# Kernel tuning notes

Hardware: AMD Instinct MI355X
Metric: run time of the kernel (lower is better)

## Reference

```python
import jax, jax.numpy as jnp
import numpy as np

EPS = 1e-8

def rmsnorm(x, w):
    norm = jax.lax.rsqrt(jnp.mean(x * x, axis=-1, keepdims=True) + EPS)
    return x * norm * w

def setup_inputs() -> dict:
    key = jax.random.key(0)
    ks = jax.random.split(key, 10)
    B, L, D, S = 8, 4096, 1024, 256
    sD = 1.0 / np.sqrt(D)
    sS = 1.0 / np.sqrt(S)
    return {
        "x": jax.random.normal(ks[0], (B, L, D), jnp.float32),
        "w_norm": jnp.ones((D,), jnp.float32),
        "W_in": jax.random.normal(ks[1], (D, 3 * S), jnp.float32) * sD,
        "b_in": jnp.zeros((3 * S,), jnp.float32),
        "W_x": jax.random.normal(ks[2], (S, S), jnp.float32) * sS,
        "b_x": jnp.zeros((S,), jnp.float32),
        "W_dt": jax.random.normal(ks[3], (S, S), jnp.float32) * sS,
        "b_dt": jnp.zeros((S,), jnp.float32),
        "W_out": jax.random.normal(ks[4], (S, D), jnp.float32) * sS,
        "b_out": jnp.zeros((D,), jnp.float32),
    }

def reference(x, w_norm, W_in, b_in, W_x, b_x, W_dt, b_dt, W_out, b_out):
    # MambaLikeBlock forward (dropout=0 / eval mode)
    residual = x
    xn = rmsnorm(x, w_norm)
    uzg = xn @ W_in + b_in                       # [B,L,3S]
    S = uzg.shape[-1] // 3
    u, z, g = uzg[..., :S], uzg[..., S:2 * S], uzg[..., 2 * S:]
    # per-step projections are time-independent -> precompute for all t
    ut = jnp.tanh(u @ W_x + b_x)                 # [B,L,S]
    dt = jax.nn.sigmoid(z @ W_dt + b_dt)         # [B,L,S]

    def step(h, inp):
        u_t, dt_t = inp
        h = (1.0 - dt_t) * h + dt_t * u_t
        return h, h

    h0 = jnp.zeros(ut.shape[::2][::-1][:0] + (ut.shape[0], ut.shape[2]), ut.dtype)  # [B,S]
    _, hs = jax.lax.scan(step, h0, (ut.transpose(1, 0, 2), dt.transpose(1, 0, 2)))
    hs = hs.transpose(1, 0, 2)                   # [B,L,S]
    y = hs * jax.nn.sigmoid(g)
    y = y @ W_out + b_out                        # [B,L,D]
    return residual + y
```

## Files before the change

kernel.cpp:

```cpp
#include <hip/hip_runtime.h>
#include <hip/hip_bf16.h>

#define BB 8
#define LL 4096
#define DD 1024
#define SS 256
#define NTOK (BB * LL)
#define CCH 64
#define TCH (LL / CCH)

typedef short bf16x8 __attribute__((ext_vector_type(8)));
typedef float f32x4 __attribute__((ext_vector_type(4)));

__device__ __forceinline__ float bfu(unsigned short v) {
  union { unsigned int i; float f; } x;
  x.i = ((unsigned int)v) << 16;
  return x.f;
}

__device__ __forceinline__ void gl_lds16(const __hip_bfloat16* g, void* l) {
  __builtin_amdgcn_global_load_lds(
      (const __attribute__((address_space(1))) unsigned int*)g,
      (__attribute__((address_space(3))) unsigned int*)l, 16, 0, 0);
}

__global__ __launch_bounds__(256) void prep_rms(const float* __restrict__ x,
                                                const float* __restrict__ wn,
                                                __hip_bfloat16* __restrict__ xn) {
  const size_t row = blockIdx.x;
  const int t = threadIdx.x;
  const float4 xv = reinterpret_cast<const float4*>(x + row * DD)[t];
  const float4 wv = reinterpret_cast<const float4*>(wn)[t];
  float ss = xv.x * xv.x + xv.y * xv.y + xv.z * xv.z + xv.w * xv.w;
#pragma unroll
  for (int m = 32; m >= 1; m >>= 1) ss += __shfl_xor(ss, m);
  __shared__ float red[4];
  if ((t & 63) == 0) red[t >> 6] = ss;
  __syncthreads();
  const float tot = red[0] + red[1] + red[2] + red[3];
  const float r = rsqrtf(tot * (1.0f / DD) + 1e-8f);
  union { ushort4 u; __hip_bfloat16 h[4]; } o;
  o.h[0] = __float2bfloat16(xv.x * wv.x * r);
  o.h[1] = __float2bfloat16(xv.y * wv.y * r);
  o.h[2] = __float2bfloat16(xv.z * wv.z * r);
  o.h[3] = __float2bfloat16(xv.w * wv.w * r);
  reinterpret_cast<ushort4*>(xn + row * DD)[t] = o.u;
}

__global__ __launch_bounds__(256) void convT4(
    const float* __restrict__ W0, const float* __restrict__ W1,
    const float* __restrict__ W2, const float* __restrict__ W3,
    __hip_bfloat16* __restrict__ T0, __hip_bfloat16* __restrict__ T1,
    __hip_bfloat16* __restrict__ T2, __hip_bfloat16* __restrict__ T3) {
  const int seg = blockIdx.y;
  const int K = (seg == 0) ? DD : SS;
  const int Nw = (seg == 0) ? 768 : (seg == 3) ? DD : SS;
  const float* W = (seg == 0) ? W0 : (seg == 1) ? W1 : (seg == 2) ? W2 : W3;
  __hip_bfloat16* T = (seg == 0) ? T0 : (seg == 1) ? T1 : (seg == 2) ? T2 : T3;
  const int idx = blockIdx.x * 256 + threadIdx.x;
  if (idx >= K * Nw) return;
  const int k = idx / Nw, n = idx % Nw;
  T[(size_t)n * K + k] = __float2bfloat16(W[idx]);
}

template <int EPI>
__global__ __launch_bounds__(256, 2) void gemm_bf16(
    const __hip_bfloat16* __restrict__ A, int lda,
    const __hip_bfloat16* __restrict__ BT,
    const float* __restrict__ bias,
    void* __restrict__ Cptr, int ldc,
    const float* __restrict__ resid,
    int K,
    const __hip_bfloat16* __restrict__ BT2,
    const float* __restrict__ bias2,
    void* __restrict__ Cptr2) {
  __shared__ __align__(16) char ldsA[2][128 * 128];
  __shared__ __align__(16) char ldsB[2][128 * 128];

  const int t = threadIdx.x;
  const int bm = blockIdx.x;
  const int bn = blockIdx.y;
  const int wave = t >> 6, lane = t & 63;
  const int wr = (wave >> 1) * 64;
  const int wc = (wave & 1) * 64;
  const int lr = lane & 15;
  const int kg = lane >> 4;
  const int rsw = lr & 7;

  const int which = (EPI == 4) ? (bn >> 1) : 0;
  const int bneff = (EPI == 4) ? (bn & 1) : bn;
  const __hip_bfloat16* Aeff = (EPI == 4 && which) ? A + SS : A;
  const __hip_bfloat16* BTeff = (EPI == 4 && which) ? BT2 : BT;
  const float* biaseff = (EPI == 4 && which) ? bias2 : bias;
  void* Ceff = (EPI == 4 && which) ? Cptr2 : Cptr;

  const int srow = lane >> 3;
  const int sg = (lane & 7) ^ srow;
  const int g_row = wave * 32 + srow;
  const __hip_bfloat16* Ab = Aeff + (size_t)(bm * 128 + g_row) * lda + sg * 8;
  const __hip_bfloat16* Bb = BTeff + (size_t)(bneff * 128 + g_row) * K + sg * 8;

  f32x4 acc[4][4] = {};

#define STAGE(d, koff)                                                        \
  {                                                                           \
    _Pragma("unroll") for (int p = 0; p < 4; ++p) {                           \
      gl_lds16(Ab + (size_t)(p * 8) * lda + (koff),                           \
               ldsA[d] + (wave * 32 + p * 8) * 128);                          \
      gl_lds16(Bb + (size_t)(p * 8) * K + (koff),                             \
               ldsB[d] + (wave * 32 + p * 8) * 128);                          \
    }                                                                         \
  }

  const int NT = K >> 6;
  STAGE(0, 0);

  for (int ti = 0; ti < NT; ++ti) {
    const int cur = ti & 1;
    if (ti + 1 < NT) {
      STAGE(cur ^ 1, (ti + 1) * 64);
      asm volatile("s_waitcnt vmcnt(8)" ::: "memory");
    } else {
      asm volatile("s_waitcnt vmcnt(0)" ::: "memory");
    }
    __builtin_amdgcn_sched_barrier(0);
    __builtin_amdgcn_s_barrier();
#pragma unroll
    for (int kh = 0; kh < 2; ++kh) {
      bf16x8 af[4], bfr[4];
#pragma unroll
      for (int m = 0; m < 4; ++m) {
        const int row = wr + m * 16 + lr;
        const int slot = (kg + kh * 4) ^ rsw;
        af[m] = *reinterpret_cast<const bf16x8*>(ldsA[cur] + row * 128 + slot * 16);
      }
#pragma unroll
      for (int n = 0; n < 4; ++n) {
        const int row = wc + n * 16 + lr;
        const int slot = (kg + kh * 4) ^ rsw;
        bfr[n] = *reinterpret_cast<const bf16x8*>(ldsB[cur] + row * 128 + slot * 16);
      }
#pragma unroll
      for (int m = 0; m < 4; ++m)
#pragma unroll
        for (int n = 0; n < 4; ++n)
          acc[m][n] = __builtin_amdgcn_mfma_f32_16x16x32_bf16(bfr[n], af[m],
                                                              acc[m][n], 0, 0, 0);
    }
    __builtin_amdgcn_sched_barrier(0);
    __builtin_amdgcn_s_barrier();
  }
#undef STAGE

  const int row0 = bm * 128 + wr + lr;
  const int col0 = bneff * 128 + wc + kg * 4;

  if (EPI == 3) {
    f32x4 rv[4][4];
    f32x4 bv[4];
#pragma unroll
    for (int n = 0; n < 4; ++n)
      bv[n] = *reinterpret_cast<const f32x4*>(&bias[col0 + n * 16]);
#pragma unroll
    for (int m = 0; m < 4; ++m) {
      const size_t rowoff = (size_t)(row0 + m * 16) * ldc;
#pragma unroll
      for (int n = 0; n < 4; ++n) {
        rv[m][n] = __builtin_nontemporal_load(
            reinterpret_cast<const f32x4*>(&resid[rowoff + col0 + n * 16]));
      }
    }
    __builtin_amdgcn_sched_barrier(0);
#pragma unroll
    for (int m = 0; m < 4; ++m) {
      const size_t rowoff = (size_t)(row0 + m * 16) * ldc;
#pragma unroll
      for (int n = 0; n < 4; ++n) {
        f32x4 ov = acc[m][n] + bv[n] + rv[m][n];
        *reinterpret_cast<f32x4*>(&((float*)Cptr)[rowoff + col0 + n * 16]) = ov;
      }
    }
  } else {
#pragma unroll
    for (int m = 0; m < 4; ++m) {
      const int row = row0 + m * 16;
#pragma unroll
      for (int n = 0; n < 4; ++n) {
        const int colb = col0 + n * 16;
        const float4 bvv = *reinterpret_cast<const float4*>(&biaseff[colb]);
        float v0 = acc[m][n][0] + bvv.x;
        float v1 = acc[m][n][1] + bvv.y;
        float v2 = acc[m][n][2] + bvv.z;
        float v3 = acc[m][n][3] + bvv.w;
        if (EPI == 1 || (EPI == 4 && which == 0)) {
          v0 = tanhf(v0); v1 = tanhf(v1); v2 = tanhf(v2); v3 = tanhf(v3);
        } else if (EPI == 2 || (EPI == 4 && which == 1)) {
          v0 = 1.f / (1.f + expf(-v0)); v1 = 1.f / (1.f + expf(-v1));
          v2 = 1.f / (1.f + expf(-v2)); v3 = 1.f / (1.f + expf(-v3));
        }
        union { ushort4 u; __hip_bfloat16 h[4]; } o;
        o.h[0] = __float2bfloat16(v0); o.h[1] = __float2bfloat16(v1);
        o.h[2] = __float2bfloat16(v2); o.h[3] = __float2bfloat16(v3);
        *reinterpret_cast<ushort4*>(
            &((__hip_bfloat16*)Ceff)[(size_t)row * ldc + colb]) = o.u;
      }
    }
  }
}

__global__ __launch_bounds__(128) void scan_phase_a(
    const __hip_bfloat16* __restrict__ ut,
    const __hip_bfloat16* __restrict__ dtb,
    float* __restrict__ h0s, float* __restrict__ As) {
  const int bc = blockIdx.x;
  const int b = bc / CCH, c = bc % CCH;
  const int ch = threadIdx.x * 2;
  const size_t base = ((size_t)b * LL + (size_t)c * TCH) * SS + ch;
  float h0 = 0.f, h1 = 0.f, A0 = 1.f, A1 = 1.f;
#pragma unroll 8
  for (int t = 0; t < TCH; ++t) {
    const ushort2 uu = *reinterpret_cast<const ushort2*>(ut + base + (size_t)t * SS);
    const ushort2 dd = *reinterpret_cast<const ushort2*>(dtb + base + (size_t)t * SS);
    const float d0 = bfu(dd.x), d1 = bfu(dd.y);
    h0 = fmaf(d0, bfu(uu.x) - h0, h0);
    h1 = fmaf(d1, bfu(uu.y) - h1, h1);
    A0 *= (1.f - d0);
    A1 *= (1.f - d1);
  }
  const size_t o = (size_t)bc * SS + ch;
  *reinterpret_cast<float2*>(h0s + o) = make_float2(h0, h1);
  *reinterpret_cast<float2*>(As + o) = make_float2(A0, A1);
}

__global__ __launch_bounds__(256) void scan_phase_b(
    const float* __restrict__ h0s, const float* __restrict__ As,
    float* __restrict__ hins) {
  const int b = blockIdx.x;
  const int s = threadIdx.x;
  float hin = 0.f;
#pragma unroll 8
  for (int c = 0; c < CCH; ++c) {
    const size_t idx = ((size_t)b * CCH + c) * SS + s;
    hins[idx] = hin;
    hin = fmaf(As[idx], hin, h0s[idx]);
  }
}

__global__ __launch_bounds__(128) void scan_phase_c(
    const __hip_bfloat16* __restrict__ ut,
    const __hip_bfloat16* __restrict__ dtb,
    const __hip_bfloat16* __restrict__ gz,
    const float* __restrict__ hins,
    __hip_bfloat16* __restrict__ hsg) {
  const int bc = blockIdx.x;
  const int b = bc / CCH, c = bc % CCH;
  const int ch = threadIdx.x * 2;
  const size_t rowbase = (size_t)b * LL + (size_t)c * TCH;
  const float2 hv = *reinterpret_cast<const float2*>(hins + (size_t)bc * SS + ch);
  float h0 = hv.x, h1 = hv.y;
#pragma unroll 8
  for (int t = 0; t < TCH; ++t) {
    const size_t row = rowbase + t;
    const ushort2 uu = *reinterpret_cast<const ushort2*>(ut + row * SS + ch);
    const ushort2 dd = *reinterpret_cast<const ushort2*>(dtb + row * SS + ch);
    const ushort2 gg = *reinterpret_cast<const ushort2*>(gz + row * 768 + ch);
    h0 = fmaf(bfu(dd.x), bfu(uu.x) - h0, h0);
    h1 = fmaf(bfu(dd.y), bfu(uu.y) - h1, h1);
    union { ushort2 u; __hip_bfloat16 h[2]; } o;
    o.h[0] = __float2bfloat16(h0 / (1.f + expf(-bfu(gg.x))));
    o.h[1] = __float2bfloat16(h1 / (1.f + expf(-bfu(gg.y))));
    *reinterpret_cast<ushort2*>(hsg + row * SS + ch) = o.u;
  }
}

extern "C" void kernel_launch(void* const* d_in, const int* in_sizes, int n_in,
                              void* d_out, int out_size, void* d_ws, size_t ws_size,
                              hipStream_t stream) {
  const float* x      = (const float*)d_in[0];
  const float* w_norm = (const float*)d_in[1];
  const float* W_in   = (const float*)d_in[2];
  const float* b_in   = (const float*)d_in[3];
  const float* W_x    = (const float*)d_in[4];
  const float* b_x    = (const float*)d_in[5];
  const float* W_dt   = (const float*)d_in[6];
  const float* b_dt   = (const float*)d_in[7];
  const float* W_out  = (const float*)d_in[8];
  const float* b_out  = (const float*)d_in[9];
  float* out = (float*)d_out;

  char* w = (char*)d_ws;
  __hip_bfloat16* xn  = (__hip_bfloat16*)w;
  __hip_bfloat16* ut  = (__hip_bfloat16*)w;
  __hip_bfloat16* dtb = (__hip_bfloat16*)(w + (size_t)NTOK * SS * 2);
  w += (size_t)NTOK * DD * 2;
  __hip_bfloat16* uzg = (__hip_bfloat16*)w;  w += (size_t)NTOK * 768 * 2;
  __hip_bfloat16* WinT  = (__hip_bfloat16*)w;  w += (size_t)768 * DD * 2;
  __hip_bfloat16* WxT   = (__hip_bfloat16*)w;  w += (size_t)SS * SS * 2;
  __hip_bfloat16* WdtT  = (__hip_bfloat16*)w;  w += (size_t)SS * SS * 2;
  __hip_bfloat16* WoutT = (__hip_bfloat16*)w;  w += (size_t)DD * SS * 2;
  float* h0s  = (float*)w;  w += (size_t)BB * CCH * SS * 4;
  float* As   = (float*)w;  w += (size_t)BB * CCH * SS * 4;
  float* hins = (float*)w;  w += (size_t)BB * CCH * SS * 4;
  (void)ws_size; (void)n_in; (void)in_sizes; (void)out_size;

  convT4<<<dim3((DD * 768 + 255) / 256, 4), 256, 0, stream>>>(
      W_in, W_x, W_dt, W_out, WinT, WxT, WdtT, WoutT);

  prep_rms<<<NTOK, 256, 0, stream>>>(x, w_norm, xn);

  gemm_bf16<0><<<dim3(NTOK / 128, 768 / 128), 256, 0, stream>>>(
      xn, DD, WinT, b_in, uzg, 768, nullptr, DD, nullptr, nullptr, nullptr);

  gemm_bf16<4><<<dim3(NTOK / 128, 4), 256, 0, stream>>>(
      uzg, 768, WxT, b_x, ut, SS, nullptr, SS, WdtT, b_dt, dtb);

  scan_phase_a<<<BB * CCH, 128, 0, stream>>>(ut, dtb, h0s, As);
  scan_phase_b<<<BB, 256, 0, stream>>>(h0s, As, hins);
  scan_phase_c<<<BB * CCH, 128, 0, stream>>>(ut, dtb, uzg + 2 * SS, hins, ut);

  gemm_bf16<3><<<dim3(NTOK / 128, DD / 128), 256, 0, stream>>>(
      ut, SS, WoutT, b_out, out, DD, x, SS, nullptr, nullptr, nullptr);
}
```

Measured before the change: 275.4 us.

## Switch GEMM to 4-stage K=32 LDS pipeline with three tiles in flight

```diff
diff --git a/kernel.cpp b/kernel.cpp
--- a/kernel.cpp
+++ b/kernel.cpp
@@ -74,8 +74,8 @@
     const __hip_bfloat16* __restrict__ BT2,
     const float* __restrict__ bias2,
     void* __restrict__ Cptr2) {
-  __shared__ __align__(16) char ldsA[2][128 * 128];
-  __shared__ __align__(16) char ldsB[2][128 * 128];
+  __shared__ __align__(16) char ldsA[4 * 8192];
+  __shared__ __align__(16) char ldsB[4 * 8192];
 
   const int t = threadIdx.x;
   const int bm = blockIdx.x;
@@ -85,7 +85,7 @@
   const int wc = (wave & 1) * 64;
   const int lr = lane & 15;
   const int kg = lane >> 4;
-  const int rsw = lr & 7;
+  const int rkey = (lr >> 1) & 3;
 
   const int which = (EPI == 4) ? (bn >> 1) : 0;
   const int bneff = (EPI == 4) ? (bn & 1) : bn;
@@ -94,59 +94,63 @@
   const float* biaseff = (EPI == 4 && which) ? bias2 : bias;
   void* Ceff = (EPI == 4 && which) ? Cptr2 : Cptr;
 
-  const int srow = lane >> 3;
-  const int sg = (lane & 7) ^ srow;
-  const int g_row = wave * 32 + srow;
-  const __hip_bfloat16* Ab = Aeff + (size_t)(bm * 128 + g_row) * lda + sg * 8;
-  const __hip_bfloat16* Bb = BTeff + (size_t)(bneff * 128 + g_row) * K + sg * 8;
+  const int sg = (lane & 3) ^ ((lane >> 3) & 3);
+  const int s_row = wave * 32 + (lane >> 2);
+  const __hip_bfloat16* Ab = Aeff + (size_t)(bm * 128 + s_row) * lda + sg * 8;
+  const __hip_bfloat16* Bb = BTeff + (size_t)(bneff * 128 + s_row) * K + sg * 8;
 
   f32x4 acc[4][4] = {};
 
 #define STAGE(d, koff)                                                        \
   {                                                                           \
-    _Pragma("unroll") for (int p = 0; p < 4; ++p) {                           \
-      gl_lds16(Ab + (size_t)(p * 8) * lda + (koff),                           \
-               ldsA[d] + (wave * 32 + p * 8) * 128);                          \
-      gl_lds16(Bb + (size_t)(p * 8) * K + (koff),                             \
-               ldsB[d] + (wave * 32 + p * 8) * 128);                          \
+    _Pragma("unroll") for (int p = 0; p < 2; ++p) {                           \
+      gl_lds16(Ab + (size_t)(p * 16) * lda + (koff),                          \
+               ldsA + (d) * 8192 + (wave * 32 + p * 16) * 64);                \
+      gl_lds16(Bb + (size_t)(p * 16) * K + (koff),                            \
+               ldsB + (d) * 8192 + (wave * 32 + p * 16) * 64);                \
     }                                                                         \
   }
 
-  const int NT = K >> 6;
+  const int NT = K >> 5;
   STAGE(0, 0);
+  STAGE(1, 32);
+  STAGE(2, 64);
 
   for (int ti = 0; ti < NT; ++ti) {
-    const int cur = ti & 1;
-    if (ti + 1 < NT) {
-      STAGE(cur ^ 1, (ti + 1) * 64);
+    if (ti + 3 < NT) {
+      STAGE((ti + 3) & 3, (ti + 3) * 32);
+      asm volatile("s_waitcnt vmcnt(12)" ::: "memory");
+    } else if (ti + 2 < NT) {
       asm volatile("s_waitcnt vmcnt(8)" ::: "memory");
+    } else if (ti + 1 < NT) {
+      asm volatile("s_waitcnt vmcnt(4)" ::: "memory");
     } else {
       asm volatile("s_waitcnt vmcnt(0)" ::: "memory");
     }
     __builtin_amdgcn_sched_barrier(0);
     __builtin_amdgcn_s_barrier();
-#pragma unroll
-    for (int kh = 0; kh < 2; ++kh) {
-      bf16x8 af[4], bfr[4];
-#pragma unroll
-      for (int m = 0; m < 4; ++m) {
-        const int row = wr + m * 16 + lr;
-        const int slot = (kg + kh * 4) ^ rsw;
-        af[m] = *reinterpret_cast<const bf16x8*>(ldsA[cur] + row * 128 + slot * 16);
-      }
-#pragma unroll
-      for (int n = 0; n < 4; ++n) {
-        const int row = wc + n * 16 + lr;
-        const int slot = (kg + kh * 4) ^ rsw;
-        bfr[n] = *reinterpret_cast<const bf16x8*>(ldsB[cur] + row * 128 + slot * 16);
-      }
-#pragma unroll
-      for (int m = 0; m < 4; ++m)
-#pragma unroll
-        for (int n = 0; n < 4; ++n)
-          acc[m][n] = __builtin_amdgcn_mfma_f32_16x16x32_bf16(bfr[n], af[m],
-                                                              acc[m][n], 0, 0, 0);
-    }
+
+    const char* bufA = ldsA + (ti & 3) * 8192;
+    const char* bufB = ldsB + (ti & 3) * 8192;
+    bf16x8 af[4], bfr[4];
+#pragma unroll
+    for (int m = 0; m < 4; ++m) {
+      const int row = wr + m * 16 + lr;
+      const int slot = kg ^ rkey;
+      af[m] = *reinterpret_cast<const bf16x8*>(bufA + row * 64 + slot * 16);
+    }
+#pragma unroll
+    for (int n = 0; n < 4; ++n) {
+      const int row = wc + n * 16 + lr;
+      const int slot = kg ^ rkey;
+      bfr[n] = *reinterpret_cast<const bf16x8*>(bufB + row * 64 + slot * 16);
+    }
+#pragma unroll
+    for (int m = 0; m < 4; ++m)
+#pragma unroll
+      for (int n = 0; n < 4; ++n)
+        acc[m][n] = __builtin_amdgcn_mfma_f32_16x16x32_bf16(bfr[n], af[m],
+                                                            acc[m][n], 0, 0, 0);
     __builtin_amdgcn_sched_barrier(0);
     __builtin_amdgcn_s_barrier();
   }
```

Measured after the change: 287.6 us. 4.4% more time.

## Add dedicated 8-wave 256x128 triple-buffered GEMM for input projection

Applied to the files above, without the earlier changes.

```diff
diff --git a/kernel.cpp b/kernel.cpp
--- a/kernel.cpp
+++ b/kernel.cpp
@@ -61,6 +61,175 @@
   if (idx >= K * Nw) return;
   const int k = idx / Nw, n = idx % Nw;
   T[(size_t)n * K + k] = __float2bfloat16(W[idx]);
+}
+
+__global__ __launch_bounds__(512, 2) void gemm0_8p(
+    const __hip_bfloat16* __restrict__ A,
+    const __hip_bfloat16* __restrict__ BT,
+    const float* __restrict__ bias,
+    __hip_bfloat16* __restrict__ C) {
+  __shared__ __align__(16) char ldsA[3 * 32768];
+  __shared__ __align__(16) char ldsB[3 * 16384];
+
+  const int t = threadIdx.x;
+  const int bm = blockIdx.x, bn = blockIdx.y;
+  const int wave = t >> 6, lane = t & 63;
+  const int wm = wave >> 1, wn = wave & 1;
+  const int wr = wm * 64, wc = wn * 64;
+  const int lr = lane & 15;
+  const int kg = lane >> 4;
+  const int rsw = lr & 7;
+
+  const int srow = lane >> 3;
+  const int sg = (lane & 7) ^ srow;
+  const __hip_bfloat16* Abase = A + (size_t)(bm * 256) * DD + sg * 8;
+  const __hip_bfloat16* Bbase = BT + (size_t)(bn * 128) * DD + sg * 8;
+
+  f32x4 acc[4][4] = {};
+
+#define STA(buf, h, p, koff)                                                  \
+  gl_lds16(Abase + (size_t)((h)*128 + wave * 16 + (p)*8 + srow) * DD + (koff),\
+           ldsA + (buf)*32768 + ((h)*128 + wave * 16 + (p)*8) * 128)
+#define STB(buf, p, koff)                                                     \
+  gl_lds16(Bbase + (size_t)(wave * 16 + (p)*8 + srow) * DD + (koff),          \
+           ldsB + (buf)*16384 + (wave * 16 + (p)*8) * 128)
+#define LDA_(row, slot) \
+  (*reinterpret_cast<const bf16x8*>(bufA + (row)*128 + (slot)*16))
+#define LDB_(row, slot) \
+  (*reinterpret_cast<const bf16x8*>(bufB + (row)*128 + (slot)*16))
+
+  const int NT = DD / 64;
+#pragma unroll
+  for (int p = 0; p < 2; ++p) {
+    STA(0, 0, p, 0); STA(0, 1, p, 0); STB(0, p, 0);
+  }
+#pragma unroll
+  for (int p = 0; p < 2; ++p) {
+    STA(1, 0, p, 64); STA(1, 1, p, 64); STB(1, p, 64);
+  }
+
+  for (int ti = 0; ti < NT; ++ti) {
+    if (ti < NT - 1) {
+      asm volatile("s_waitcnt vmcnt(6)" ::: "memory");
+    } else {
+      asm volatile("s_waitcnt vmcnt(0)" ::: "memory");
+    }
+    __builtin_amdgcn_sched_barrier(0);
+    __builtin_amdgcn_s_barrier();
+
+    const int cb = ti % 3;
+    const int sb = (ti + 2) % 3;
+    const bool st = (ti + 2) < NT;
+    const int koff = (ti + 2) * 64;
+    const char* bufA = ldsA + cb * 32768;
+    const char* bufB = ldsB + cb * 16384;
+
+    bf16x8 a0, a1, a2, a3, b0, b1, b2, b3;
+    {
+      const int s0 = kg ^ rsw;
+      a0 = LDA_(wr + 0 * 16 + lr, s0);
+      a1 = LDA_(wr + 1 * 16 + lr, s0);
+      b0 = LDB_(wc + 0 * 16 + lr, s0);
+      b1 = LDB_(wc + 1 * 16 + lr, s0);
+      b2 = LDB_(wc + 2 * 16 + lr, s0);
+      b3 = LDB_(wc + 3 * 16 + lr, s0);
+      if (st) { STA(sb, 0, 0, koff); STA(sb, 0, 1, koff); }
+      asm volatile("s_waitcnt lgkmcnt(0)" ::: "memory");
+      __builtin_amdgcn_sched_barrier(0);
+      __builtin_amdgcn_s_setprio(1);
+      acc[0][0] = __builtin_amdgcn_mfma_f32_16x16x32_bf16(b0, a0, acc[0][0], 0, 0, 0);
+      acc[0][1] = __builtin_amdgcn_mfma_f32_16x16x32_bf16(b1, a0, acc[0][1], 0, 0, 0);
+      acc[0][2] = __builtin_amdgcn_mfma_f32_16x16x32_bf16(b2, a0, acc[0][2], 0, 0, 0);
+      acc[0][3] = __builtin_amdgcn_mfma_f32_16x16x32_bf16(b3, a0, acc[0][3], 0, 0, 0);
+      acc[1][0] = __builtin_amdgcn_mfma_f32_16x16x32_bf16(b0, a1, acc[1][0], 0, 0, 0);
+      acc[1][1] = __builtin_amdgcn_mfma_f32_16x16x32_bf16(b1, a1, acc[1][1], 0, 0, 0);
+      acc[1][2] = __builtin_amdgcn_mfma_f32_16x16x32_bf16(b2, a1, acc[1][2], 0, 0, 0);
+      acc[1][3] = __builtin_amdgcn_mfma_f32_16x16x32_bf16(b3, a1, acc[1][3], 0, 0, 0);
+      __builtin_amdgcn_s_setprio(0);
+      __builtin_amdgcn_s_barrier();
+    }
+    {
+      const int s0 = kg ^ rsw;
+      a2 = LDA_(wr + 2 * 16 + lr, s0);
+      a3 = LDA_(wr + 3 * 16 + lr, s0);
+      if (st) { STA(sb, 1, 0, koff); STA(sb, 1, 1, koff); }
+      asm volatile("s_waitcnt lgkmcnt(0)" ::: "memory");
+      __builtin_amdgcn_sched_barrier(0);
+      __builtin_amdgcn_s_setprio(1);
+      acc[2][0] = __builtin_amdgcn_mfma_f32_16x16x32_bf16(b0, a2, acc[2][0], 0, 0, 0);
+      acc[2][1] = __builtin_amdgcn_mfma_f32_16x16x32_bf16(b1, a2, acc[2][1], 0, 0, 0);
+      acc[2][2] = __builtin_amdgcn_mfma_f32_16x16x32_bf16(b2, a2, acc[2][2], 0, 0, 0);
+      acc[2][3] = __builtin_amdgcn_mfma_f32_16x16x32_bf16(b3, a2, acc[2][3], 0, 0, 0);
+      acc[3][0] = __builtin_amdgcn_mfma_f32_16x16x32_bf16(b0, a3, acc[3][0], 0, 0, 0);
+      acc[3][1] = __builtin_amdgcn_mfma_f32_16x16x32_bf16(b1, a3, acc[3][1], 0, 0, 0);
+      acc[3][2] = __builtin_amdgcn_mfma_f32_16x16x32_bf16(b2, a3, acc[3][2], 0, 0, 0);
+      acc[3][3] = __builtin_amdgcn_mfma_f32_16x16x32_bf16(b3, a3, acc[3][3], 0, 0, 0);
+      __builtin_amdgcn_s_setprio(0);
+      __builtin_amdgcn_s_barrier();
+    }
+    {
+      const int s1 = (kg + 4) ^ rsw;
+      a0 = LDA_(wr + 0 * 16 + lr, s1);
+      a1 = LDA_(wr + 1 * 16 + lr, s1);
+      b0 = LDB_(wc + 0 * 16 + lr, s1);
+      b1 = LDB_(wc + 1 * 16 + lr, s1);
+      b2 = LDB_(wc + 2 * 16 + lr, s1);
+      b3 = LDB_(wc + 3 * 16 + lr, s1);
+      if (st) { STB(sb, 0, koff); STB(sb, 1, koff); }
+      asm volatile("s_waitcnt lgkmcnt(0)" ::: "memory");
+      __builtin_amdgcn_sched_barrier(0);
+      __builtin_amdgcn_s_setprio(1);
+      acc[0][0] = __builtin_amdgcn_mfma_f32_16x16x32_bf16(b0, a0, acc[0][0], 0, 0, 0);
+      acc[0][1] = __builtin_amdgcn_mfma_f32_16x16x32_bf16(b1, a0, acc[0][1], 0, 0, 0);
+      acc[0][2] = __builtin_amdgcn_mfma_f32_16x16x32_bf16(b2, a0, acc[0][2], 0, 0, 0);
+      acc[0][3] = __builtin_amdgcn_mfma_f32_16x16x32_bf16(b3, a0, acc[0][3], 0, 0, 0);
+      acc[1][0] = __builtin_amdgcn_mfma_f32_16x16x32_bf16(b0, a1, acc[1][0], 0, 0, 0);
+      acc[1][1] = __builtin_amdgcn_mfma_f32_16x16x32_bf16(b1, a1, acc[1][1], 0, 0, 0);
+      acc[1][2] = __builtin_amdgcn_mfma_f32_16x16x32_bf16(b2, a1, acc[1][2], 0, 0, 0);
+      acc[1][3] = __builtin_amdgcn_mfma_f32_16x16x32_bf16(b3, a1, acc[1][3], 0, 0, 0);
+      __builtin_amdgcn_s_setprio(0);
+      __builtin_amdgcn_s_barrier();
+    }
+    {
+      const int s1 = (kg + 4) ^ rsw;
+      a2 = LDA_(wr + 2 * 16 + lr, s1);
+      a3 = LDA_(wr + 3 * 16 + lr, s1);
+      asm volatile("s_waitcnt lgkmcnt(0)" ::: "memory");
+      __builtin_amdgcn_sched_barrier(0);
+      __builtin_amdgcn_s_setprio(1);
+      acc[2][0] = __builtin_amdgcn_mfma_f32_16x16x32_bf16(b0, a2, acc[2][0], 0, 0, 0);
+      acc[2][1] = __builtin_amdgcn_mfma_f32_16x16x32_bf16(b1, a2, acc[2][1], 0, 0, 0);
+      acc[2][2] = __builtin_amdgcn_mfma_f32_16x16x32_bf16(b2, a2, acc[2][2], 0, 0, 0);
+      acc[2][3] = __builtin_amdgcn_mfma_f32_16x16x32_bf16(b3, a2, acc[2][3], 0, 0, 0);
+      acc[3][0] = __builtin_amdgcn_mfma_f32_16x16x32_bf16(b0, a3, acc[3][0], 0, 0, 0);
+      acc[3][1] = __builtin_amdgcn_mfma_f32_16x16x32_bf16(b1, a3, acc[3][1], 0, 0, 0);
+      acc[3][2] = __builtin_amdgcn_mfma_f32_16x16x32_bf16(b2, a3, acc[3][2], 0, 0, 0);
+      acc[3][3] = __builtin_amdgcn_mfma_f32_16x16x32_bf16(b3, a3, acc[3][3], 0, 0, 0);
+      __builtin_amdgcn_s_setprio(0);
+    }
+  }
+#undef STA
+#undef STB
+#undef LDA_
+#undef LDB_
+
+  const int row0 = bm * 256 + wr + lr;
+  const int col0 = bn * 128 + wc + kg * 4;
+#pragma unroll
+  for (int m = 0; m < 4; ++m) {
+    const int row = row0 + m * 16;
+#pragma unroll
+    for (int n = 0; n < 4; ++n) {
+      const int colb = col0 + n * 16;
+      const float4 bv = *reinterpret_cast<const float4*>(&bias[colb]);
+      union { ushort4 u; __hip_bfloat16 h[4]; } o;
+      o.h[0] = __float2bfloat16(acc[m][n][0] + bv.x);
+      o.h[1] = __float2bfloat16(acc[m][n][1] + bv.y);
+      o.h[2] = __float2bfloat16(acc[m][n][2] + bv.z);
+      o.h[3] = __float2bfloat16(acc[m][n][3] + bv.w);
+      *reinterpret_cast<ushort4*>(&C[(size_t)row * 768 + colb]) = o.u;
+    }
+  }
 }
 
 template <int EPI>
@@ -308,8 +477,8 @@
 
   prep_rms<<<NTOK, 256, 0, stream>>>(x, w_norm, xn);
 
-  gemm_bf16<0><<<dim3(NTOK / 128, 768 / 128), 256, 0, stream>>>(
-      xn, DD, WinT, b_in, uzg, 768, nullptr, DD, nullptr, nullptr, nullptr);
+  gemm0_8p<<<dim3(NTOK / 256, 768 / 128), 512, 0, stream>>>(
+      xn, WinT, b_in, uzg);
 
   gemm_bf16<4><<<dim3(NTOK / 128, 4), 256, 0, stream>>>(
       uzg, 768, WxT, b_x, ut, SS, nullptr, SS, WdtT, b_dt, dtb);
```

Result: slower. 285.8 us (+3.8%).
